# Optimization experiments

Hardware: AMD Instinct MI355X
Metric: run time of the kernel (lower is better)

## Reference

```python
import jax, jax.numpy as jnp
import numpy as np

NUM_HEADS = 8
GROUPS = 32  # min(32, 512 // 4)
EPS = 1e-5


def group_norm(y, gamma, beta):
    B, C, L = y.shape
    yg = y.reshape(B, GROUPS, -1)  # [B, G, (C//G)*L]
    mu = yg.mean(-1, keepdims=True)
    var = yg.var(-1, keepdims=True)
    yn = ((yg - mu) * jax.lax.rsqrt(var + EPS)).reshape(B, C, L)
    return yn * gamma[:, None] + beta[:, None]


def setup_inputs() -> dict:
    key = jax.random.key(0)
    ks = jax.random.split(key, 5)
    B, C, L = 4, 512, 2048
    return {
        "x": jax.random.normal(ks[0], (B, C, L), dtype=jnp.float32),
        "Wqkv": jax.random.normal(ks[1], (3 * C, C), dtype=jnp.float32) * (C ** -0.5),
        "bqkv": jax.random.normal(ks[2], (3 * C,), dtype=jnp.float32) * 0.01,
        "Wproj": jax.random.normal(ks[3], (C, C), dtype=jnp.float32) * (C ** -0.5),
        "bproj": jax.random.normal(ks[4], (C,), dtype=jnp.float32) * 0.01,
        "gamma": jnp.ones((C,), dtype=jnp.float32),
        "beta": jnp.zeros((C,), dtype=jnp.float32),
    }


def reference(x, Wqkv, bqkv, Wproj, bproj, gamma, beta):
    B, C, L = x.shape
    H = NUM_HEADS
    D = C // H
    # 1x1 Conv1d == channel-mixing matmul
    qkv = jnp.einsum('oc,bcl->bol', Wqkv, x) + bqkv[:, None]  # [B, 3C, L]
    qkv = qkv.reshape(B, 3, H, D, L)
    q, k, v = qkv[:, 0], qkv[:, 1], qkv[:, 2]
    q = jnp.clip(q, -10.0, 10.0)
    k = jnp.clip(k, -10.0, 10.0)
    v = jnp.clip(v, -10.0, 10.0)
    scale = D ** -0.5
    attn = jnp.einsum('bhdi,bhdj->bhij', q, k) * scale  # [B, H, L, L]
    attn = jnp.clip(attn, -10.0, 10.0)
    attn = jax.nn.softmax(attn, axis=-1)
    # NaN fallback: replace whole attn with identity if any NaN (matches torch branch)
    has_nan = jnp.isnan(attn).any()
    attn = jnp.where(has_nan, jnp.eye(L, dtype=x.dtype), attn)
    out = jnp.einsum('bhij,bhdj->bhdi', attn, v)  # [B, H, D, L]
    out = out.reshape(B, C, L)
    out = jnp.einsum('oc,bcl->bol', Wproj, out) + bproj[:, None]
    return group_norm(out + x, gamma, beta)
```

## Files before the change

### kernel.cpp

```cpp
#include <hip/hip_runtime.h>
#include <cstddef>

#define B_ 4
#define C_ 512
#define L_ 2048

typedef __attribute__((ext_vector_type(8))) short  short8;
typedef __attribute__((ext_vector_type(4))) float  f32x4;
typedef __attribute__((ext_vector_type(4))) unsigned short us4;

#define AS1 __attribute__((address_space(1)))
#define AS3 __attribute__((address_space(3)))

__device__ __forceinline__ float clip10(float v){ return fminf(fmaxf(v,-10.0f),10.0f); }

__device__ __forceinline__ unsigned short f2bf(float f){
  union { float f; unsigned u; } v; v.f = f;
  unsigned r = v.u + 0x7fffu + ((v.u >> 16) & 1u);
  return (unsigned short)(r >> 16);
}
__device__ __forceinline__ unsigned pk_tr(float lo, float hi){
  return __builtin_amdgcn_perm(__float_as_uint(hi), __float_as_uint(lo), 0x07060302u);
}
__device__ __forceinline__ float bf2f(unsigned short u){
  return __uint_as_float(((unsigned)u)<<16);
}
__device__ __forceinline__ void gl16(const void* g, void* l){
  __builtin_amdgcn_global_load_lds((const AS1 unsigned*)g, (AS3 unsigned*)l, 16, 0, 0);
}
__device__ __forceinline__ void drain_dma(){
  asm volatile("s_waitcnt vmcnt(0)" ::: "memory");
}
__device__ __forceinline__ short8 mk8(unsigned a, unsigned b, unsigned c, unsigned d){
  union { unsigned u[4]; short8 s; } v;
  v.u[0]=a; v.u[1]=b; v.u[2]=c; v.u[3]=d;
  return v.s;
}

__global__ __launch_bounds__(256) void prep_k(
    const float* __restrict__ x, const float* __restrict__ Wq,
    const float* __restrict__ Wp, unsigned short* __restrict__ xT,
    unsigned short* __restrict__ Wqb, unsigned short* __restrict__ Wpb,
    float* __restrict__ part)
{
  const int blk = blockIdx.x;
  const int t = threadIdx.x;
  if (blk < 4096){
    __shared__ float tile[32][33];
    const int b = blk>>10, rem = blk&1023;
    const int c0 = (rem>>6)*32, l0 = (rem&63)*32;
    const int cr = t>>3, lc = (t&7)*4;
    const float4 v = *(const float4*)(x + ((size_t)b*C_ + c0+cr)*L_ + l0 + lc);
    tile[cr][lc]=v.x; tile[cr][lc+1]=v.y; tile[cr][lc+2]=v.z; tile[cr][lc+3]=v.w;
    __syncthreads();
    const int lr = t>>3, cc = (t&7)*4;
    const us4 o = { f2bf(tile[cc][lr]), f2bf(tile[cc+1][lr]),
                    f2bf(tile[cc+2][lr]), f2bf(tile[cc+3][lr]) };
    *(us4*)(xT + ((size_t)b*L_ + l0+lr)*C_ + c0 + cc) = o;
  } else if (blk < 5120){
    const int i = (blk-4096)*256 + t;
    const int NQ = 1536*512/4;
    const float* src; unsigned short* dst; int j;
    if (i < NQ){ src = Wq; dst = Wqb; j = i; }
    else       { src = Wp; dst = Wpb; j = i - NQ; }
    const float4 v = *(const float4*)(src + (size_t)j*4);
    const us4 o = { f2bf(v.x), f2bf(v.y), f2bf(v.z), f2bf(v.w) };
    *(us4*)(dst + (size_t)j*4) = o;
  } else {
    part[t] = 0.f;
  }
}

template<int MODE>
__global__ __launch_bounds__(256) void mfma_gemm(
    const unsigned short* __restrict__ Wb, const unsigned short* __restrict__ Bin,
    const float* __restrict__ bias, const float* __restrict__ xres,
    unsigned short* __restrict__ qT, unsigned short* __restrict__ kT,
    unsigned short* __restrict__ vN, float* __restrict__ yout,
    float* __restrict__ part)
{
  __shared__ unsigned short SA[128*64];
  __shared__ unsigned short SB[128*64];
  const int t = threadIdx.x;
  const int b = blockIdx.z;
  const int mb = blockIdx.y, n0 = blockIdx.x*128, m0 = mb*128;
  const int lane = t&63, w = t>>6, wm = w>>1, wn = w&1;
  const int n = lane&15, q4 = lane>>4;
  const bool VSWAP = (MODE==0) && (mb>=8);

  f32x4 acc[4][4];
#pragma unroll
  for (int i=0;i<4;i++)
#pragma unroll
    for (int j=0;j<4;j++) acc[i][j] = (f32x4){0.f,0.f,0.f,0.f};

  const unsigned short* Arow = Wb + (size_t)m0*512;
  const unsigned short* Brow = Bin + ((size_t)b*L_ + n0)*512;

  for (int kt=0; kt<8; kt++){
    const int k0 = kt*64;
    __syncthreads();
#pragma unroll
    for (int i=0;i<4;i++){
      const int ch = t + 256*i;
      const int row = ch>>3, lc = (ch&7) ^ (row&7);
      gl16(Arow + (size_t)row*512 + k0 + lc*8, &SA[ch*8]);
      gl16(Brow + (size_t)row*512 + k0 + lc*8, &SB[ch*8]);
    }
    drain_dma();
    __syncthreads();
#pragma unroll
    for (int kk=0;kk<2;kk++){
      short8 aF[4], bF[4];
      const int pc = ((kk*4+q4) ^ (n&7))*8;
#pragma unroll
      for (int mt=0;mt<4;mt++) aF[mt] = *(const short8*)&SA[(wm*64+mt*16+n)*64 + pc];
#pragma unroll
      for (int nt=0;nt<4;nt++) bF[nt] = *(const short8*)&SB[(wn*64+nt*16+n)*64 + pc];
      if (VSWAP){
#pragma unroll
        for (int mt=0;mt<4;mt++)
#pragma unroll
          for (int nt=0;nt<4;nt++)
            acc[mt][nt] = __builtin_amdgcn_mfma_f32_16x16x32_bf16(bF[nt], aF[mt], acc[mt][nt], 0,0,0);
      } else {
#pragma unroll
        for (int mt=0;mt<4;mt++)
#pragma unroll
          for (int nt=0;nt<4;nt++)
            acc[mt][nt] = __builtin_amdgcn_mfma_f32_16x16x32_bf16(aF[mt], bF[nt], acc[mt][nt], 0,0,0);
      }
    }
  }

  const float QS = 0.180336880f;
  if (VSWAP){
#pragma unroll
    for (int mt=0;mt<4;mt++){
      const int o = m0 + wm*64 + mt*16 + n;
      const float bv = bias[o];
#pragma unroll
      for (int nt=0;nt<4;nt++){
        const int p = ((nt>>1)<<2) | ((q4&1)<<3) | ((q4>>1)<<4) | ((nt&1)<<5);
        const int l = n0 + wn*64 + p;
        const float r0=clip10(acc[mt][nt][0]+bv), r1=clip10(acc[mt][nt][1]+bv),
                    r2=clip10(acc[mt][nt][2]+bv), r3=clip10(acc[mt][nt][3]+bv);
        const us4 ov = { f2bf(r0), f2bf(r1), f2bf(r2), f2bf(r3) };
        *(us4*)&vN[((size_t)b*512 + (o-1024))*L_ + l] = ov;
      }
    }
    return;
  }
#pragma unroll
  for (int mt=0;mt<4;mt++){
    const int obase = m0 + wm*64 + mt*16 + q4*4;
    const float b0=bias[obase], b1=bias[obase+1], b2=bias[obase+2], b3=bias[obase+3];
    float gs=0.f, gq=0.f;
#pragma unroll
    for (int nt=0;nt<4;nt++){
      const int l = n0 + wn*64 + nt*16 + n;
      float r0=acc[mt][nt][0]+b0, r1=acc[mt][nt][1]+b1,
            r2=acc[mt][nt][2]+b2, r3=acc[mt][nt][3]+b3;
      if (MODE==0){
        r0=clip10(r0); r1=clip10(r1); r2=clip10(r2); r3=clip10(r3);
        const int typ = mb>>2;
        const int oin = obase - typ*512;
        if (typ==0){ r0*=QS; r1*=QS; r2*=QS; r3*=QS; }
        unsigned short* dst = (typ==0) ? qT : kT;
        const us4 o = { f2bf(r0), f2bf(r1), f2bf(r2), f2bf(r3) };
        *(us4*)&dst[((size_t)b*L_ + l)*512 + oin] = o;
      } else {
        const float* xp = xres + ((size_t)b*512 + obase)*L_ + l;
        const float y0=r0+xp[0], y1=r1+xp[(size_t)L_],
                    y2=r2+xp[(size_t)2*L_], y3=r3+xp[(size_t)3*L_];
        float* dst = yout + ((size_t)b*512 + obase)*L_ + l;
        dst[0]=y0; dst[(size_t)L_]=y1; dst[(size_t)2*L_]=y2; dst[(size_t)3*L_]=y3;
        gs += (y0+y1)+(y2+y3);
        gq += (y0*y0+y1*y1)+(y2*y2+y3*y3);
      }
    }
    if (MODE==1){
#pragma unroll
      for (int off=1; off<64; off<<=1){
        gs += __shfl_xor(gs, off);
        gq += __shfl_xor(gq, off);
      }
      if (lane==0){
        const int g = mb*8 + wm*4 + mt;
        atomicAdd(&part[(b*32+g)*2+0], gs);
        atomicAdd(&part[(b*32+g)*2+1], gq);
      }
    }
  }
}

#define OPX 68

__global__ __launch_bounds__(256,4) void attn_v10(
    const unsigned short* __restrict__ qT, const unsigned short* __restrict__ kT,
    const unsigned short* __restrict__ vN,
    unsigned short* __restrict__ Opart, float* __restrict__ den)
{
  __shared__ unsigned short smem[16384];
  const int t  = threadIdx.x;
  const int io = blockIdx.x>>1, half = blockIdx.x&1;
  const int i0 = io*128;
  const int h  = blockIdx.y, b = blockIdx.z;
  const int lane = t&63, w = t>>6, n = lane&15, q4 = lane>>4;
  const int idx = ((b*8+h)*16+io)*2 + half;

  const unsigned short* kb0 = kT + (size_t)b*L_*512 + h*64;
  const unsigned short* vb  = vN + ((size_t)b*512 + h*64)*L_;

  short8 qf[2][2];
#pragma unroll
  for (int mt=0; mt<2; mt++)
#pragma unroll
    for (int kk=0; kk<2; kk++)
      qf[mt][kk] = *(const short8*)(qT + ((size_t)b*L_ + i0 + w*32 + mt*16 + n)*512
                                       + h*64 + kk*32 + q4*8);

  short8 ones;
#pragma unroll
  for (int i=0;i<8;i++) ones[i] = (short)0x3F80;

  f32x4 oacc[2][4];
  f32x4 oden[2];
#pragma unroll
  for (int mt=0;mt<2;mt++){ oden[mt]=(f32x4){0.f,0.f,0.f,0.f};
#pragma unroll
    for (int dt=0;dt<4;dt++) oacc[mt][dt]=(f32x4){0.f,0.f,0.f,0.f}; }

  const float LIM = 14.4269504089f;
  const int jbeg = half*1024, jend = jbeg+1024;

#pragma unroll
  for (int i=0;i<2;i++){
    const int ch = t + 256*i, row = ch>>3, lc = (ch&7)^(row&7);
    gl16(kb0 + (size_t)(jbeg+row)*512 + lc*8, &smem[ch*8]);
    gl16(vb  + (size_t)row*L_ + jbeg + lc*8,  &smem[4096 + ch*8]);
  }
  drain_dma();
  __syncthreads();

  for (int j0=jbeg; j0<jend; j0+=64){
    const int cur = ((j0-jbeg)>>6)&1;
    const unsigned short* sk = &smem[cur*8192];
    const unsigned short* sv = &smem[cur*8192 + 4096];

    if (j0+64 < jend){
      const int nb = cur^1;
#pragma unroll
      for (int i=0;i<2;i++){
        const int ch = t + 256*i, row = ch>>3, lc = (ch&7)^(row&7);
        gl16(kb0 + (size_t)(j0+64+row)*512 + lc*8, &smem[nb*8192 + ch*8]);
        gl16(vb  + (size_t)row*L_ + j0+64 + lc*8,  &smem[nb*8192+4096 + ch*8]);
      }
    }

    f32x4 sacc[2][4];
#pragma unroll
    for (int mt=0;mt<2;mt++)
#pragma unroll
      for (int jt=0;jt<4;jt++) sacc[mt][jt]=(f32x4){0.f,0.f,0.f,0.f};
#pragma unroll
    for (int kk=0;kk<2;kk++){
      const int pc = ((kk*4+q4) ^ (n&7))*8;
      short8 aK[4];
#pragma unroll
      for (int jt=0;jt<4;jt++) aK[jt] = *(const short8*)&sk[(jt*16+n)*64 + pc];
#pragma unroll
      for (int mt=0;mt<2;mt++)
#pragma unroll
        for (int jt=0;jt<4;jt++)
          sacc[mt][jt] = __builtin_amdgcn_mfma_f32_16x16x32_bf16(aK[jt], qf[mt][kk], sacc[mt][jt], 0,0,0);
    }

    unsigned pw[2][4][2];
#pragma unroll
    for (int mt=0;mt<2;mt++)
#pragma unroll
      for (int jt=0;jt<4;jt++){
        const float e0 = __builtin_amdgcn_exp2f(__builtin_amdgcn_fmed3f(sacc[mt][jt][0],-LIM,LIM));
        const float e1 = __builtin_amdgcn_exp2f(__builtin_amdgcn_fmed3f(sacc[mt][jt][1],-LIM,LIM));
        const float e2 = __builtin_amdgcn_exp2f(__builtin_amdgcn_fmed3f(sacc[mt][jt][2],-LIM,LIM));
        const float e3 = __builtin_amdgcn_exp2f(__builtin_amdgcn_fmed3f(sacc[mt][jt][3],-LIM,LIM));
        pw[mt][jt][0] = pk_tr(e0,e1);
        pw[mt][jt][1] = pk_tr(e2,e3);
      }

#pragma unroll
    for (int kk=0;kk<2;kk++){
      const int pcv = ((kk*4+q4) ^ (n&7))*8;
      short8 bV[4];
#pragma unroll
      for (int dt=0;dt<4;dt++) bV[dt] = *(const short8*)&sv[(dt*16+n)*64 + pcv];
#pragma unroll
      for (int mt=0;mt<2;mt++){
        const short8 pA = mk8(pw[mt][kk][0], pw[mt][kk][1],
                              pw[mt][kk+2][0], pw[mt][kk+2][1]);
#pragma unroll
        for (int dt=0;dt<4;dt++)
          oacc[mt][dt] = __builtin_amdgcn_mfma_f32_16x16x32_bf16(pA, bV[dt], oacc[mt][dt], 0,0,0);
        oden[mt] = __builtin_amdgcn_mfma_f32_16x16x32_bf16(pA, ones, oden[mt], 0,0,0);
      }
    }
    drain_dma();
    __syncthreads();
  }

  if (n == 0){
#pragma unroll
    for (int mt=0;mt<2;mt++)
#pragma unroll
      for (int r=0;r<4;r++)
        den[(size_t)idx*128 + w*32 + mt*16 + q4*4 + r] = oden[mt][r];
  }

  unsigned short* sb = smem;
#pragma unroll
  for (int mt=0;mt<2;mt++)
#pragma unroll
    for (int dt=0;dt<4;dt++)
#pragma unroll
      for (int r=0;r<4;r++)
        sb[(w*32 + mt*16 + q4*4 + r)*OPX + dt*16 + n] = f2bf(oacc[mt][dt][r]);
#pragma unroll
  for (int it=0; it<8; it++){
    const int chunk = it*64 + lane;
    const int row = chunk>>4, c4 = (chunk&15)*4;
    const us4 ov = *(const us4*)&sb[(w*32 + row)*OPX + c4];
    *(us4*)&Opart[(size_t)idx*8192 + (w*32 + row)*64 + c4] = ov;
  }
}

__global__ __launch_bounds__(256) void attn_combine(
    const unsigned short* __restrict__ Opart, const float* __restrict__ den,
    unsigned short* __restrict__ attnT)
{
  __shared__ float s_inv[128];
  const int io = blockIdx.x, h = blockIdx.y, b = blockIdx.z;
  const int t = threadIdx.x;
  const int base = ((b*8+h)*16+io)*2;
  if (t < 128)
    s_inv[t] = 1.0f/(den[(size_t)base*128 + t] + den[(size_t)(base+1)*128 + t]);
  __syncthreads();
  const unsigned short* O0 = Opart + (size_t)base*8192;
  const unsigned short* O1 = O0 + 8192;
#pragma unroll
  for (int it=0; it<8; it++){
    const int chunk = it*256 + t;
    const int i = chunk>>4, c4 = (chunk&15)*4;
    const us4 a = *(const us4*)&O0[i*64 + c4];
    const us4 c = *(const us4*)&O1[i*64 + c4];
    const float inv = s_inv[i];
    const us4 o = { f2bf((bf2f(a[0])+bf2f(c[0]))*inv),
                    f2bf((bf2f(a[1])+bf2f(c[1]))*inv),
                    f2bf((bf2f(a[2])+bf2f(c[2]))*inv),
                    f2bf((bf2f(a[3])+bf2f(c[3]))*inv) };
    *(us4*)&attnT[((size_t)b*L_ + io*128 + i)*512 + h*64 + c4] = o;
  }
}

__global__ __launch_bounds__(256) void gn_apply(
    const float* __restrict__ y, const float* __restrict__ part,
    const float* __restrict__ gamma, const float* __restrict__ beta,
    float* __restrict__ out)
{
  const int blk = blockIdx.x;
  const int b = blk>>7, g = (blk>>2)&31, s = blk&3;
  const float sum = part[(b*32+g)*2+0];
  const float sq  = part[(b*32+g)*2+1];
  const float mu = sum*(1.0f/32768.0f);
  const float rs = rsqrtf(sq*(1.0f/32768.0f) - mu*mu + 1e-5f);
  const size_t base = ((size_t)b*C_ + g*16)*L_ + s*512;
  const int t = threadIdx.x;
#pragma unroll
  for (int i=0;i<8;i++){
    const int e = i*256 + t;
    const int row = e>>7;
    const size_t off = base + (size_t)row*L_ + (e&127)*4;
    const int c = g*16 + row;
    const float ga = gamma[c], be = beta[c];
    const float4 vy=*(const float4*)(y+off);
    float4 r;
    r.x=(vy.x-mu)*rs*ga+be;
    r.y=(vy.y-mu)*rs*ga+be;
    r.z=(vy.z-mu)*rs*ga+be;
    r.w=(vy.w-mu)*rs*ga+be;
    *(float4*)(out+off)=r;
  }
}

extern "C" void kernel_launch(void* const* d_in, const int* in_sizes, int n_in,
                              void* d_out, int out_size, void* d_ws, size_t ws_size,
                              hipStream_t stream)
{
  (void)in_sizes; (void)n_in; (void)out_size; (void)ws_size;
  const float* x     = (const float*)d_in[0];
  const float* Wqkv  = (const float*)d_in[1];
  const float* bqkv  = (const float*)d_in[2];
  const float* Wproj = (const float*)d_in[3];
  const float* bproj = (const float*)d_in[4];
  const float* gamma = (const float*)d_in[5];
  const float* beta  = (const float*)d_in[6];
  float* out = (float*)d_out;
  char* ws = (char*)d_ws;

  const size_t MB = 1024*1024;
  unsigned short* qT    = (unsigned short*)(ws);
  unsigned short* kT    = (unsigned short*)(ws +  8*MB);
  unsigned short* vN    = (unsigned short*)(ws + 16*MB);
  unsigned short* attnT = (unsigned short*)(ws + 24*MB);
  unsigned short* xT    = (unsigned short*)(ws + 32*MB);
  float*          den   = (float*)        (ws + 41*MB);
  unsigned short* Wqb   = (unsigned short*)(ws + 42*MB);
  unsigned short* Wpb   = (unsigned short*)(ws + 44*MB);
  float*          y     = (float*)        (ws + 45*MB);
  unsigned short* Opart = (unsigned short*)(ws + 45*MB);
  float*          part  = (float*)        (ws + 61*MB);

  prep_k      <<<dim3(5121),   256,0,stream>>>(x, Wqkv, Wproj, xT, Wqb, Wpb, part);
  mfma_gemm<0><<<dim3(16,12,4),256,0,stream>>>(Wqb, xT,    bqkv , nullptr, qT,kT,vN, nullptr, nullptr);
  attn_v10    <<<dim3(32,8,4), 256,0,stream>>>(qT, kT, vN, Opart, den);
  attn_combine<<<dim3(16,8,4), 256,0,stream>>>(Opart, den, attnT);
  mfma_gemm<1><<<dim3(16, 4,4),256,0,stream>>>(Wpb, attnT, bproj, x, nullptr,nullptr,nullptr, y, part);
  gn_apply    <<<dim3(512),    256,0,stream>>>(y, part, gamma, beta, out);
}
```

Measured before the change: 182.2 us.

## Double-buffer LDS in projection GEMM and raise MFMA priority in attention

Adds a templated double-buffered path to the MFMA GEMM that prefetches the next K tile into an alternate LDS buffer while computing the current one. Only the output-projection GEMM uses it; the QKV GEMM keeps single buffering. It also wraps the QK and PV MFMA sections of the attention kernel in s_setprio so matrix work gets scheduling priority over other waves. Double buffering doubles LDS use in the projection GEMM, which can lower occupancy.

```diff
diff --git a/kernel.cpp b/kernel.cpp
--- a/kernel.cpp
+++ b/kernel.cpp
@@ -71,7 +71,7 @@
   }
 }
 
-template<int MODE>
+template<int MODE, int DBUF>
 __global__ __launch_bounds__(256) void mfma_gemm(
     const unsigned short* __restrict__ Wb, const unsigned short* __restrict__ Bin,
     const float* __restrict__ bias, const float* __restrict__ xres,
@@ -79,8 +79,8 @@
     unsigned short* __restrict__ vN, float* __restrict__ yout,
     float* __restrict__ part)
 {
-  __shared__ unsigned short SA[128*64];
-  __shared__ unsigned short SB[128*64];
+  __shared__ unsigned short SA[(1+DBUF)*128*64];
+  __shared__ unsigned short SB[(1+DBUF)*128*64];
   const int t = threadIdx.x;
   const int b = blockIdx.z;
   const int mb = blockIdx.y, n0 = blockIdx.x*128, m0 = mb*128;
@@ -97,26 +97,55 @@
   const unsigned short* Arow = Wb + (size_t)m0*512;
   const unsigned short* Brow = Bin + ((size_t)b*L_ + n0)*512;
 
-  for (int kt=0; kt<8; kt++){
-    const int k0 = kt*64;
-    __syncthreads();
+  if (DBUF){
 #pragma unroll
     for (int i=0;i<4;i++){
       const int ch = t + 256*i;
       const int row = ch>>3, lc = (ch&7) ^ (row&7);
-      gl16(Arow + (size_t)row*512 + k0 + lc*8, &SA[ch*8]);
-      gl16(Brow + (size_t)row*512 + k0 + lc*8, &SB[ch*8]);
+      gl16(Arow + (size_t)row*512 + lc*8, &SA[ch*8]);
+      gl16(Brow + (size_t)row*512 + lc*8, &SB[ch*8]);
     }
     drain_dma();
     __syncthreads();
+  }
+
+  for (int kt=0; kt<8; kt++){
+    const int k0 = kt*64;
+    int cur = 0;
+    if (!DBUF){
+      __syncthreads();
+#pragma unroll
+      for (int i=0;i<4;i++){
+        const int ch = t + 256*i;
+        const int row = ch>>3, lc = (ch&7) ^ (row&7);
+        gl16(Arow + (size_t)row*512 + k0 + lc*8, &SA[ch*8]);
+        gl16(Brow + (size_t)row*512 + k0 + lc*8, &SB[ch*8]);
+      }
+      drain_dma();
+      __syncthreads();
+    } else {
+      cur = kt&1;
+      if (kt < 7){
+        const int nb = cur^1;
+#pragma unroll
+        for (int i=0;i<4;i++){
+          const int ch = t + 256*i;
+          const int row = ch>>3, lc = (ch&7) ^ (row&7);
+          gl16(Arow + (size_t)row*512 + k0+64 + lc*8, &SA[nb*8192 + ch*8]);
+          gl16(Brow + (size_t)row*512 + k0+64 + lc*8, &SB[nb*8192 + ch*8]);
+        }
+      }
+    }
+    const unsigned short* sA = &SA[cur*8192];
+    const unsigned short* sB = &SB[cur*8192];
 #pragma unroll
     for (int kk=0;kk<2;kk++){
       short8 aF[4], bF[4];
       const int pc = ((kk*4+q4) ^ (n&7))*8;
 #pragma unroll
-      for (int mt=0;mt<4;mt++) aF[mt] = *(const short8*)&SA[(wm*64+mt*16+n)*64 + pc];
-#pragma unroll
-      for (int nt=0;nt<4;nt++) bF[nt] = *(const short8*)&SB[(wn*64+nt*16+n)*64 + pc];
+      for (int mt=0;mt<4;mt++) aF[mt] = *(const short8*)&sA[(wm*64+mt*16+n)*64 + pc];
+#pragma unroll
+      for (int nt=0;nt<4;nt++) bF[nt] = *(const short8*)&sB[(wn*64+nt*16+n)*64 + pc];
       if (VSWAP){
 #pragma unroll
         for (int mt=0;mt<4;mt++)
@@ -130,6 +159,10 @@
           for (int nt=0;nt<4;nt++)
             acc[mt][nt] = __builtin_amdgcn_mfma_f32_16x16x32_bf16(aF[mt], bF[nt], acc[mt][nt], 0,0,0);
       }
+    }
+    if (DBUF && kt < 7){
+      drain_dma();
+      __syncthreads();
     }
   }
 
@@ -263,6 +296,7 @@
     for (int mt=0;mt<2;mt++)
 #pragma unroll
       for (int jt=0;jt<4;jt++) sacc[mt][jt]=(f32x4){0.f,0.f,0.f,0.f};
+    __builtin_amdgcn_s_setprio(1);
 #pragma unroll
     for (int kk=0;kk<2;kk++){
       const int pc = ((kk*4+q4) ^ (n&7))*8;
@@ -275,6 +309,7 @@
         for (int jt=0;jt<4;jt++)
           sacc[mt][jt] = __builtin_amdgcn_mfma_f32_16x16x32_bf16(aK[jt], qf[mt][kk], sacc[mt][jt], 0,0,0);
     }
+    __builtin_amdgcn_s_setprio(0);
 
     unsigned pw[2][4][2];
 #pragma unroll
@@ -289,6 +324,7 @@
         pw[mt][jt][1] = pk_tr(e2,e3);
       }
 
+    __builtin_amdgcn_s_setprio(1);
 #pragma unroll
     for (int kk=0;kk<2;kk++){
       const int pcv = ((kk*4+q4) ^ (n&7))*8;
@@ -305,6 +341,7 @@
         oden[mt] = __builtin_amdgcn_mfma_f32_16x16x32_bf16(pA, ones, oden[mt], 0,0,0);
       }
     }
+    __builtin_amdgcn_s_setprio(0);
     drain_dma();
     __syncthreads();
   }
@@ -420,10 +457,10 @@
   unsigned short* Opart = (unsigned short*)(ws + 45*MB);
   float*          part  = (float*)        (ws + 61*MB);
 
-  prep_k      <<<dim3(5121),   256,0,stream>>>(x, Wqkv, Wproj, xT, Wqb, Wpb, part);
-  mfma_gemm<0><<<dim3(16,12,4),256,0,stream>>>(Wqb, xT,    bqkv , nullptr, qT,kT,vN, nullptr, nullptr);
-  attn_v10    <<<dim3(32,8,4), 256,0,stream>>>(qT, kT, vN, Opart, den);
-  attn_combine<<<dim3(16,8,4), 256,0,stream>>>(Opart, den, attnT);
-  mfma_gemm<1><<<dim3(16, 4,4),256,0,stream>>>(Wpb, attnT, bproj, x, nullptr,nullptr,nullptr, y, part);
-  gn_apply    <<<dim3(512),    256,0,stream>>>(y, part, gamma, beta, out);
-}
+  prep_k        <<<dim3(5121),   256,0,stream>>>(x, Wqkv, Wproj, xT, Wqb, Wpb, part);
+  mfma_gemm<0,0><<<dim3(16,12,4),256,0,stream>>>(Wqb, xT,    bqkv , nullptr, qT,kT,vN, nullptr, nullptr);
+  attn_v10      <<<dim3(32,8,4), 256,0,stream>>>(qT, kT, vN, Opart, den);
+  attn_combine  <<<dim3(16,8,4), 256,0,stream>>>(Opart, den, attnT);
+  mfma_gemm<1,1><<<dim3(16, 4,4),256,0,stream>>>(Wpb, attnT, bproj, x, nullptr,nullptr,nullptr, y, part);
+  gn_apply      <<<dim3(512),    256,0,stream>>>(y, part, gamma, beta, out);
+}
```

New measurement: 186.3 us. 1.02x slower.

## Drop key-split attention and fuse normalization into the attention kernel

Applied to the files above, without the earlier changes.

The attention kernel no longer splits the key range into two halves with a separate combine kernel. Each block now handles 64 query rows (16 per wave) over all 2048 keys, divides by the softmax denominator in registers, and writes bf16 output directly to attnT. This removes the combine launch and the round-trip of partial outputs and denominators through global memory. In exchange, each K/V tile loaded into LDS feeds only one query sub-tile per wave instead of two, so K/V traffic and LDS reads per MFMA double, and each block runs a serial loop twice as long.

```diff
diff --git a/kernel.cpp b/kernel.cpp
--- a/kernel.cpp
+++ b/kernel.cpp
@@ -196,59 +196,52 @@
 
 #define OPX 68
 
-__global__ __launch_bounds__(256,4) void attn_v10(
+__global__ __launch_bounds__(256,4) void attn_v11(
     const unsigned short* __restrict__ qT, const unsigned short* __restrict__ kT,
     const unsigned short* __restrict__ vN,
-    unsigned short* __restrict__ Opart, float* __restrict__ den)
+    unsigned short* __restrict__ attnT)
 {
   __shared__ unsigned short smem[16384];
   const int t  = threadIdx.x;
-  const int io = blockIdx.x>>1, half = blockIdx.x&1;
-  const int i0 = io*128;
+  const int i0 = blockIdx.x*64;
   const int h  = blockIdx.y, b = blockIdx.z;
   const int lane = t&63, w = t>>6, n = lane&15, q4 = lane>>4;
-  const int idx = ((b*8+h)*16+io)*2 + half;
 
   const unsigned short* kb0 = kT + (size_t)b*L_*512 + h*64;
   const unsigned short* vb  = vN + ((size_t)b*512 + h*64)*L_;
 
-  short8 qf[2][2];
-#pragma unroll
-  for (int mt=0; mt<2; mt++)
-#pragma unroll
-    for (int kk=0; kk<2; kk++)
-      qf[mt][kk] = *(const short8*)(qT + ((size_t)b*L_ + i0 + w*32 + mt*16 + n)*512
-                                       + h*64 + kk*32 + q4*8);
+  short8 qf[2];
+#pragma unroll
+  for (int kk=0; kk<2; kk++)
+    qf[kk] = *(const short8*)(qT + ((size_t)b*L_ + i0 + w*16 + n)*512
+                                 + h*64 + kk*32 + q4*8);
 
   short8 ones;
 #pragma unroll
   for (int i=0;i<8;i++) ones[i] = (short)0x3F80;
 
-  f32x4 oacc[2][4];
-  f32x4 oden[2];
-#pragma unroll
-  for (int mt=0;mt<2;mt++){ oden[mt]=(f32x4){0.f,0.f,0.f,0.f};
-#pragma unroll
-    for (int dt=0;dt<4;dt++) oacc[mt][dt]=(f32x4){0.f,0.f,0.f,0.f}; }
+  f32x4 oacc[4];
+  f32x4 oden = (f32x4){0.f,0.f,0.f,0.f};
+#pragma unroll
+  for (int dt=0;dt<4;dt++) oacc[dt]=(f32x4){0.f,0.f,0.f,0.f};
 
   const float LIM = 14.4269504089f;
-  const int jbeg = half*1024, jend = jbeg+1024;
 
 #pragma unroll
   for (int i=0;i<2;i++){
     const int ch = t + 256*i, row = ch>>3, lc = (ch&7)^(row&7);
-    gl16(kb0 + (size_t)(jbeg+row)*512 + lc*8, &smem[ch*8]);
-    gl16(vb  + (size_t)row*L_ + jbeg + lc*8,  &smem[4096 + ch*8]);
+    gl16(kb0 + (size_t)row*512 + lc*8, &smem[ch*8]);
+    gl16(vb  + (size_t)row*L_ + lc*8,  &smem[4096 + ch*8]);
   }
   drain_dma();
   __syncthreads();
 
-  for (int j0=jbeg; j0<jend; j0+=64){
-    const int cur = ((j0-jbeg)>>6)&1;
+  for (int j0=0; j0<L_; j0+=64){
+    const int cur = (j0>>6)&1;
     const unsigned short* sk = &smem[cur*8192];
     const unsigned short* sv = &smem[cur*8192 + 4096];
 
-    if (j0+64 < jend){
+    if (j0+64 < L_){
       const int nb = cur^1;
 #pragma unroll
       for (int i=0;i<2;i++){
@@ -258,11 +251,9 @@
       }
     }
 
-    f32x4 sacc[2][4];
-#pragma unroll
-    for (int mt=0;mt<2;mt++)
-#pragma unroll
-      for (int jt=0;jt<4;jt++) sacc[mt][jt]=(f32x4){0.f,0.f,0.f,0.f};
+    f32x4 sacc[4];
+#pragma unroll
+    for (int jt=0;jt<4;jt++) sacc[jt]=(f32x4){0.f,0.f,0.f,0.f};
 #pragma unroll
     for (int kk=0;kk<2;kk++){
       const int pc = ((kk*4+q4) ^ (n&7))*8;
@@ -270,24 +261,20 @@
 #pragma unroll
       for (int jt=0;jt<4;jt++) aK[jt] = *(const short8*)&sk[(jt*16+n)*64 + pc];
 #pragma unroll
-      for (int mt=0;mt<2;mt++)
-#pragma unroll
-        for (int jt=0;jt<4;jt++)
-          sacc[mt][jt] = __builtin_amdgcn_mfma_f32_16x16x32_bf16(aK[jt], qf[mt][kk], sacc[mt][jt], 0,0,0);
-    }
-
-    unsigned pw[2][4][2];
-#pragma unroll
-    for (int mt=0;mt<2;mt++)
-#pragma unroll
-      for (int jt=0;jt<4;jt++){
-        const float e0 = __builtin_amdgcn_exp2f(__builtin_amdgcn_fmed3f(sacc[mt][jt][0],-LIM,LIM));
-        const float e1 = __builtin_amdgcn_exp2f(__builtin_amdgcn_fmed3f(sacc[mt][jt][1],-LIM,LIM));
-        const float e2 = __builtin_amdgcn_exp2f(__builtin_amdgcn_fmed3f(sacc[mt][jt][2],-LIM,LIM));
-        const float e3 = __builtin_amdgcn_exp2f(__builtin_amdgcn_fmed3f(sacc[mt][jt][3],-LIM,LIM));
-        pw[mt][jt][0] = pk_tr(e0,e1);
-        pw[mt][jt][1] = pk_tr(e2,e3);
-      }
+      for (int jt=0;jt<4;jt++)
+        sacc[jt] = __builtin_amdgcn_mfma_f32_16x16x32_bf16(aK[jt], qf[kk], sacc[jt], 0,0,0);
+    }
+
+    unsigned pw[4][2];
+#pragma unroll
+    for (int jt=0;jt<4;jt++){
+      const float e0 = __builtin_amdgcn_exp2f(__builtin_amdgcn_fmed3f(sacc[jt][0],-LIM,LIM));
+      const float e1 = __builtin_amdgcn_exp2f(__builtin_amdgcn_fmed3f(sacc[jt][1],-LIM,LIM));
+      const float e2 = __builtin_amdgcn_exp2f(__builtin_amdgcn_fmed3f(sacc[jt][2],-LIM,LIM));
+      const float e3 = __builtin_amdgcn_exp2f(__builtin_amdgcn_fmed3f(sacc[jt][3],-LIM,LIM));
+      pw[jt][0] = pk_tr(e0,e1);
+      pw[jt][1] = pk_tr(e2,e3);
+    }
 
 #pragma unroll
     for (int kk=0;kk<2;kk++){
@@ -295,70 +282,32 @@
       short8 bV[4];
 #pragma unroll
       for (int dt=0;dt<4;dt++) bV[dt] = *(const short8*)&sv[(dt*16+n)*64 + pcv];
-#pragma unroll
-      for (int mt=0;mt<2;mt++){
-        const short8 pA = mk8(pw[mt][kk][0], pw[mt][kk][1],
-                              pw[mt][kk+2][0], pw[mt][kk+2][1]);
-#pragma unroll
-        for (int dt=0;dt<4;dt++)
-          oacc[mt][dt] = __builtin_amdgcn_mfma_f32_16x16x32_bf16(pA, bV[dt], oacc[mt][dt], 0,0,0);
-        oden[mt] = __builtin_amdgcn_mfma_f32_16x16x32_bf16(pA, ones, oden[mt], 0,0,0);
-      }
+      const short8 pA = mk8(pw[kk][0], pw[kk][1], pw[kk+2][0], pw[kk+2][1]);
+#pragma unroll
+      for (int dt=0;dt<4;dt++)
+        oacc[dt] = __builtin_amdgcn_mfma_f32_16x16x32_bf16(pA, bV[dt], oacc[dt], 0,0,0);
+      oden = __builtin_amdgcn_mfma_f32_16x16x32_bf16(pA, ones, oden, 0,0,0);
     }
     drain_dma();
     __syncthreads();
   }
 
-  if (n == 0){
-#pragma unroll
-    for (int mt=0;mt<2;mt++)
-#pragma unroll
-      for (int r=0;r<4;r++)
-        den[(size_t)idx*128 + w*32 + mt*16 + q4*4 + r] = oden[mt][r];
-  }
+  float inv[4];
+#pragma unroll
+  for (int r=0;r<4;r++) inv[r] = 1.0f/oden[r];
 
   unsigned short* sb = smem;
 #pragma unroll
-  for (int mt=0;mt<2;mt++)
-#pragma unroll
-    for (int dt=0;dt<4;dt++)
-#pragma unroll
-      for (int r=0;r<4;r++)
-        sb[(w*32 + mt*16 + q4*4 + r)*OPX + dt*16 + n] = f2bf(oacc[mt][dt][r]);
-#pragma unroll
-  for (int it=0; it<8; it++){
+  for (int dt=0;dt<4;dt++)
+#pragma unroll
+    for (int r=0;r<4;r++)
+      sb[(w*16 + q4*4 + r)*OPX + dt*16 + n] = f2bf(oacc[dt][r]*inv[r]);
+#pragma unroll
+  for (int it=0; it<4; it++){
     const int chunk = it*64 + lane;
     const int row = chunk>>4, c4 = (chunk&15)*4;
-    const us4 ov = *(const us4*)&sb[(w*32 + row)*OPX + c4];
-    *(us4*)&Opart[(size_t)idx*8192 + (w*32 + row)*64 + c4] = ov;
-  }
-}
-
-__global__ __launch_bounds__(256) void attn_combine(
-    const unsigned short* __restrict__ Opart, const float* __restrict__ den,
-    unsigned short* __restrict__ attnT)
-{
-  __shared__ float s_inv[128];
-  const int io = blockIdx.x, h = blockIdx.y, b = blockIdx.z;
-  const int t = threadIdx.x;
-  const int base = ((b*8+h)*16+io)*2;
-  if (t < 128)
-    s_inv[t] = 1.0f/(den[(size_t)base*128 + t] + den[(size_t)(base+1)*128 + t]);
-  __syncthreads();
-  const unsigned short* O0 = Opart + (size_t)base*8192;
-  const unsigned short* O1 = O0 + 8192;
-#pragma unroll
-  for (int it=0; it<8; it++){
-    const int chunk = it*256 + t;
-    const int i = chunk>>4, c4 = (chunk&15)*4;
-    const us4 a = *(const us4*)&O0[i*64 + c4];
-    const us4 c = *(const us4*)&O1[i*64 + c4];
-    const float inv = s_inv[i];
-    const us4 o = { f2bf((bf2f(a[0])+bf2f(c[0]))*inv),
-                    f2bf((bf2f(a[1])+bf2f(c[1]))*inv),
-                    f2bf((bf2f(a[2])+bf2f(c[2]))*inv),
-                    f2bf((bf2f(a[3])+bf2f(c[3]))*inv) };
-    *(us4*)&attnT[((size_t)b*L_ + io*128 + i)*512 + h*64 + c4] = o;
+    const us4 ov = *(const us4*)&sb[(w*16 + row)*OPX + c4];
+    *(us4*)&attnT[((size_t)b*L_ + i0 + w*16 + row)*512 + h*64 + c4] = ov;
   }
 }
 
@@ -413,17 +362,14 @@
   unsigned short* vN    = (unsigned short*)(ws + 16*MB);
   unsigned short* attnT = (unsigned short*)(ws + 24*MB);
   unsigned short* xT    = (unsigned short*)(ws + 32*MB);
-  float*          den   = (float*)        (ws + 41*MB);
   unsigned short* Wqb   = (unsigned short*)(ws + 42*MB);
   unsigned short* Wpb   = (unsigned short*)(ws + 44*MB);
   float*          y     = (float*)        (ws + 45*MB);
-  unsigned short* Opart = (unsigned short*)(ws + 45*MB);
   float*          part  = (float*)        (ws + 61*MB);
 
   prep_k      <<<dim3(5121),   256,0,stream>>>(x, Wqkv, Wproj, xT, Wqb, Wpb, part);
   mfma_gemm<0><<<dim3(16,12,4),256,0,stream>>>(Wqb, xT,    bqkv , nullptr, qT,kT,vN, nullptr, nullptr);
-  attn_v10    <<<dim3(32,8,4), 256,0,stream>>>(qT, kT, vN, Opart, den);
-  attn_combine<<<dim3(16,8,4), 256,0,stream>>>(Opart, den, attnT);
+  attn_v11    <<<dim3(32,8,4), 256,0,stream>>>(qT, kT, vN, attnT);
   mfma_gemm<1><<<dim3(16, 4,4),256,0,stream>>>(Wpb, attnT, bproj, x, nullptr,nullptr,nullptr, y, part);
   gn_apply    <<<dim3(512),    256,0,stream>>>(y, part, gamma, beta, out);
 }
```

After: 180.3 us. About the same (-1.0%).
